# Optimization experiments

Hardware: AMD Instinct MI355X
Metric: run time of the kernel (lower is better)

## Reference

```python
import jax, jax.numpy as jnp
import numpy as np

MESH_SIZE = 0.01
TEMP = 0.001
T = 4096
HID = (16, 16, 16)


def _triangle_mesh():
    g = np.arange(-1.0, 1.0 + 1e-9, MESH_SIZE, dtype=np.float32)  # 201 pts
    A, B = np.meshgrid(g, g, indexing='ij')  # alpha rows, beta cols
    mask = A >= B                             # Preisach triangle alpha >= beta
    return A[mask].astype(np.float32), B[mask].astype(np.float32)  # [N], [N]


def _constrain(v, lo, hi):
    return lo + (hi - lo) * jax.nn.sigmoid(v)


def setup_inputs() -> dict:
    key = jax.random.key(0)
    ks = jax.random.split(key, 12)
    alpha_np, beta_np = _triangle_mesh()
    N = alpha_np.shape[0]  # 20301

    def xavier(k, fan_in, fan_out):
        b = np.sqrt(6.0 / (fan_in + fan_out)).astype(np.float32)
        return jax.random.uniform(k, (fan_in, fan_out), jnp.float32, -b, b)

    dims = (2,) + HID + (1,)
    params = {}
    for i in range(4):
        params[f'w{i+1}'] = xavier(ks[i], dims[i], dims[i + 1])
        params[f'b{i+1}'] = jnp.zeros((dims[i + 1],), jnp.float32)

    bound = np.sqrt(6.0 / (1 + N)).astype(np.float32)  # xavier_uniform on (1,N)
    init_state_raw = jax.random.uniform(ks[10], (N,), jnp.float32, -bound, bound)

    return dict(
        x=jax.random.normal(ks[11], (T,), jnp.float32),
        alpha_raw=jnp.asarray(alpha_np),
        beta_raw=jnp.asarray(beta_np),
        init_state_raw=init_state_raw,
        m_scale_raw=jnp.asarray(1.0, jnp.float32),
        m_offset_raw=jnp.asarray(1.0, jnp.float32),
        h_scale_raw=jnp.asarray(1.0, jnp.float32),
        **params,
    )


def _get_states(x, alpha, beta, s0, temp):
    # Soft Preisach relay: switch up where u>alpha, down where u<beta, else hold.
    def step(s, u):
        up = jax.nn.sigmoid((u - alpha) / temp)
        dn = jax.nn.sigmoid((beta - u) / temp)
        s_new = up - dn + (1.0 - up) * (1.0 - dn) * s
        return s_new, s_new
    _, states = jax.lax.scan(step, s0, x)
    return states  # [T, N]


def reference(x, alpha_raw, beta_raw, init_state_raw,
              w1, b1, w2, b2, w3, b3, w4, b4,
              m_scale_raw, m_offset_raw, h_scale_raw):
    alpha = alpha_raw  # ConstrainedParameter with no bounds -> identity
    beta = beta_raw
    s0 = jnp.tanh(init_state_raw)  # BinaryParameter (soft binary)

    states = _get_states(x, alpha, beta, s0, TEMP)  # [T, N]

    mesh = jnp.stack([alpha, beta], axis=1)  # [N, 2]
    h = jax.nn.relu(mesh @ w1 + b1)
    h = jax.nn.relu(h @ w2 + b2)
    h = jax.nn.relu(h @ w3 + b3)
    density = jax.nn.sigmoid(h @ w4 + b4)  # [N, 1]
    density = density.T  # [1, N]

    m = jnp.sum(density * states, axis=-1) / jnp.sum(density, axis=-1)  # [T]

    m_scale = _constrain(m_scale_raw, 0.0, 10.0)
    m_offset = _constrain(m_offset_raw, -10.0, 10.0)
    h_scale = _constrain(h_scale_raw, 0.0, 10.0)

    out = m_scale * m + m_offset + h_scale * x  # [T]
    return out, density, states
```

## Files before the change

kernel.cpp:

```cpp
#include <hip/hip_runtime.h>
#include <math.h>

#define NM 20301
#define TT 4096
#define NC 16
#define CH 256
#define NBLK 80
#define NWAVE 4
#define NPAR (NBLK*NWAVE)
#define TPH 16
#define NPH (CH / TPH)
#define LOG2E_K 1442.69504f
#define WNEAR 26.0f

__device__ __forceinline__ void relay_step(float ka, float kb, float ku,
                                           float& aa, float& bb) {
    float z1 = fminf(ka - ku, 63.f);
    float z2 = fminf(ku - kb, 63.f);
    float e1 = __builtin_amdgcn_exp2f(z1);
    float e2 = __builtin_amdgcn_exp2f(z2);
    float p1 = 1.f + e1, p2 = 1.f + e2;
    float r  = __builtin_amdgcn_rcpf(p1 * p2);
    aa = (e2 - e1) * r;
    bb = (e1 * e2) * r;
}

__device__ __forceinline__ float wave_reduce_sum(float w) {
    #pragma unroll
    for (int off = 32; off > 0; off >>= 1)
        w += __shfl_down(w, off, 64);
    return w;
}

__global__ __launch_bounds__(256) void density_kernel(
    const float* __restrict__ alpha, const float* __restrict__ beta,
    const float* __restrict__ w1, const float* __restrict__ b1,
    const float* __restrict__ w2, const float* __restrict__ b2,
    const float* __restrict__ w3, const float* __restrict__ b3,
    const float* __restrict__ w4, const float* __restrict__ b4,
    float* __restrict__ density_out, float* __restrict__ densum_parts)
{
    int n = blockIdx.x * 256 + threadIdx.x;
    bool valid = n < NM;
    int nn = valid ? n : NM - 1;
    float a = alpha[nn], b = beta[nn];

    float h1[16], h2[16], h3[16];
    #pragma unroll
    for (int j = 0; j < 16; j++) {
        float v = fmaf(a, w1[j], fmaf(b, w1[16 + j], b1[j]));
        h1[j] = fmaxf(v, 0.f);
    }
    #pragma unroll
    for (int j = 0; j < 16; j++) {
        float v = b2[j];
        #pragma unroll
        for (int k = 0; k < 16; k++) v = fmaf(h1[k], w2[k * 16 + j], v);
        h2[j] = fmaxf(v, 0.f);
    }
    #pragma unroll
    for (int j = 0; j < 16; j++) {
        float v = b3[j];
        #pragma unroll
        for (int k = 0; k < 16; k++) v = fmaf(h2[k], w3[k * 16 + j], v);
        h3[j] = fmaxf(v, 0.f);
    }
    float v = b4[0];
    #pragma unroll
    for (int k = 0; k < 16; k++) v = fmaf(h3[k], w4[k], v);
    float d = 1.f / (1.f + __expf(-v));

    if (valid) density_out[n] = d;
    float wsum = wave_reduce_sum(valid ? d : 0.f);
    __shared__ float ws_[NWAVE];
    if ((threadIdx.x & 63) == 0) ws_[threadIdx.x >> 6] = wsum;
    __syncthreads();
    if (threadIdx.x == 0)
        densum_parts[blockIdx.x] = ws_[0] + ws_[1] + ws_[2] + ws_[3];
}

__global__ __launch_bounds__(256) void chunk_compose_kernel(
    const float* __restrict__ x, const float* __restrict__ alpha,
    const float* __restrict__ beta,
    float* __restrict__ Abuf, float* __restrict__ Bbuf)
{
    __shared__ float xs[CH];
    int c = blockIdx.y;
    xs[threadIdx.x] = x[c * CH + threadIdx.x] * LOG2E_K;
    __syncthreads();

    int n = blockIdx.x * 256 + threadIdx.x;
    int nn = (n < NM) ? n : NM - 1;
    float ka = alpha[nn] * LOG2E_K;
    float kb = beta[nn] * LOG2E_K;

    float A = 0.f, B = 1.f;
    for (int p = 0; p < NPH; p++) {
        float xr[TPH];
        #pragma unroll
        for (int j = 0; j < TPH; j++) xr[j] = xs[p * TPH + j];
        #pragma unroll
        for (int j = 0; j < TPH; j++) {
            float ku = xr[j];
            float w1 = ka - ku, w2 = ku - kb;
            bool nearb = fminf(fabsf(w1), fabsf(w2)) < WNEAR;
            if (__any(nearb)) {
                float aa, bb;
                relay_step(ka, kb, ku, aa, bb);
                A = fmaf(bb, A, aa);
                B *= bb;
            } else {
                bool swu = w1 < 0.f, swd = w2 < 0.f;
                A = swu ? 1.f : (swd ? -1.f : A);
                B = (swu || swd) ? 0.f : B;
            }
        }
    }
    if (n < NM) { Abuf[c * NM + n] = A; Bbuf[c * NM + n] = B; }
}

__global__ __launch_bounds__(256) void chunk_scan_kernel(
    const float* __restrict__ init_raw,
    const float* __restrict__ Abuf, const float* __restrict__ Bbuf,
    float* __restrict__ sstart)
{
    int n = blockIdx.x * 256 + threadIdx.x;
    if (n >= NM) return;
    float s = tanhf(init_raw[n]);
    #pragma unroll
    for (int c = 0; c < NC; c++) {
        sstart[c * NM + n] = s;
        s = fmaf(Bbuf[c * NM + n], s, Abuf[c * NM + n]);
    }
}

__global__ __launch_bounds__(256) void states_kernel(
    const float* __restrict__ x, const float* __restrict__ alpha,
    const float* __restrict__ beta, const float* __restrict__ density,
    const float* __restrict__ sstart,
    float* __restrict__ states, float* __restrict__ partials)
{
    __shared__ float xs[CH];
    __shared__ float tile[NWAVE * 64 * (TPH + 1)];

    int tid = threadIdx.x;
    int c = blockIdx.y;
    xs[tid] = x[c * CH + tid] * LOG2E_K;

    int n = blockIdx.x * 256 + tid;
    bool valid = n < NM;
    int nn = valid ? n : NM - 1;
    float ka = alpha[nn] * LOG2E_K;
    float kb = beta[nn] * LOG2E_K;
    float d  = valid ? density[n] : 0.f;
    float s  = sstart[c * NM + nn];
    __syncthreads();

    int wv = tid >> 6, ln = tid & 63;
    int tl = ln & 15, h = ln >> 4;
    float* wtile = &tile[wv * 64 * (TPH + 1)];
    float* tslot = &wtile[ln * (TPH + 1)];
    float* rowp  = states + (size_t)c * CH * NM + n;
    size_t prow  = (size_t)(blockIdx.x * NWAVE + wv) * TT + c * CH;

    for (int p = 0; p < NPH; p++) {
        float xr[TPH];
        #pragma unroll
        for (int j = 0; j < TPH; j++) xr[j] = xs[p * TPH + j];
        #pragma unroll
        for (int j = 0; j < TPH; j++) {
            float ku = xr[j];
            float w1 = ka - ku, w2 = ku - kb;
            bool nearb = fminf(fabsf(w1), fabsf(w2)) < WNEAR;
            if (__any(nearb)) {
                float aa, bb;
                relay_step(ka, kb, ku, aa, bb);
                s = fmaf(bb, s, aa);
            } else {
                s = (w1 < 0.f) ? 1.f : ((w2 < 0.f) ? -1.f : s);
            }
            if (valid) rowp[(size_t)(p * TPH + j) * NM] = s;
            tslot[j] = d * s;
        }
        asm volatile("s_waitcnt lgkmcnt(0)" ::: "memory");
        float acc = 0.f;
        #pragma unroll
        for (int k = 0; k < TPH; k++)
            acc += wtile[(h * 16 + k) * (TPH + 1) + tl];
        acc += __shfl_xor(acc, 16, 64);
        acc += __shfl_xor(acc, 32, 64);
        if (ln < TPH) partials[prow + p * TPH + ln] = acc;
        asm volatile("s_waitcnt lgkmcnt(0)" ::: "memory");
    }
}

__global__ __launch_bounds__(256) void finalize_kernel(
    const float* __restrict__ x, const float* __restrict__ partials,
    const float* __restrict__ densum_parts,
    const float* __restrict__ msr, const float* __restrict__ mor,
    const float* __restrict__ hsr, float* __restrict__ out)
{
    int t = blockIdx.x * 256 + threadIdx.x;
    if (t >= TT) return;
    float acc = 0.f;
    for (int r = 0; r < NPAR; r++)
        acc += partials[(size_t)r * TT + t];
    float dsum = 0.f;
    for (int bx = 0; bx < NBLK; bx++)
        dsum += densum_parts[bx];
    float sig_ms = 1.f / (1.f + __expf(-msr[0]));
    float sig_mo = 1.f / (1.f + __expf(-mor[0]));
    float sig_hs = 1.f / (1.f + __expf(-hsr[0]));
    float m_scale  = 10.f * sig_ms;
    float m_offset = fmaf(20.f, sig_mo, -10.f);
    float h_scale  = 10.f * sig_hs;
    float m = acc / dsum;
    out[t] = fmaf(m_scale, m, m_offset) + h_scale * x[t];
}

extern "C" void kernel_launch(void* const* d_in, const int* in_sizes, int n_in,
                              void* d_out, int out_size, void* d_ws, size_t ws_size,
                              hipStream_t stream)
{
    const float* x    = (const float*)d_in[0];
    const float* alpha= (const float*)d_in[1];
    const float* beta = (const float*)d_in[2];
    const float* init = (const float*)d_in[3];
    const float* msr  = (const float*)d_in[4];
    const float* mor  = (const float*)d_in[5];
    const float* hsr  = (const float*)d_in[6];
    const float* w1   = (const float*)d_in[7];
    const float* b1   = (const float*)d_in[8];
    const float* w2   = (const float*)d_in[9];
    const float* b2   = (const float*)d_in[10];
    const float* w3   = (const float*)d_in[11];
    const float* b3   = (const float*)d_in[12];
    const float* w4   = (const float*)d_in[13];
    const float* b4   = (const float*)d_in[14];

    float* out     = (float*)d_out;
    float* density = out + TT;
    float* states  = density + NM;

    float* densum_parts = (float*)d_ws;
    float* sstart       = densum_parts + 128;
    float* partials     = sstart + NC * NM;

    float* Abuf = states;
    float* Bbuf = states + (size_t)NC * NM;

    density_kernel<<<dim3(NBLK), dim3(256), 0, stream>>>(
        alpha, beta, w1, b1, w2, b2, w3, b3, w4, b4, density, densum_parts);

    chunk_compose_kernel<<<dim3(NBLK, NC), dim3(256), 0, stream>>>(
        x, alpha, beta, Abuf, Bbuf);

    chunk_scan_kernel<<<dim3(NBLK), dim3(256), 0, stream>>>(
        init, Abuf, Bbuf, sstart);

    states_kernel<<<dim3(NBLK, NC), dim3(256), 0, stream>>>(
        x, alpha, beta, density, sstart, states, partials);

    finalize_kernel<<<dim3(TT / 256), dim3(256), 0, stream>>>(
        x, partials, densum_parts, msr, mor, hsr, out);
}
```

Baseline: 477.2 us.

## Re-split time into 256 short chunks with whole-mesh blocks for states pass

The time axis is split into 256 chunks of 16 steps instead of 16 chunks of 256. Each states block now covers one time chunk across the entire mesh, with 1024 threads holding 20 mesh points each. A row of states is written contiguously per step, and the density-weighted sum is reduced with wave shuffles instead of a shared-memory transpose. This aims to give a long-lived grid with coalesced full-row writes and fewer partials. In exchange, the chunk_scan pass becomes a 256-step sequential loop, the compose pass has many more small blocks, and the larger register arrays may lower occupancy.

```diff
diff --git a/kernel.cpp b/kernel.cpp
--- a/kernel.cpp
+++ b/kernel.cpp
@@ -3,13 +3,11 @@
 
 #define NM 20301
 #define TT 4096
-#define NC 16
-#define CH 256
+#define NCC 256
+#define CH2 16
 #define NBLK 80
-#define NWAVE 4
-#define NPAR (NBLK*NWAVE)
-#define TPH 16
-#define NPH (CH / TPH)
+#define NTH 1024
+#define KPT 20
 #define LOG2E_K 1442.69504f
 #define WNEAR 26.0f
 
@@ -72,7 +70,7 @@
 
     if (valid) density_out[n] = d;
     float wsum = wave_reduce_sum(valid ? d : 0.f);
-    __shared__ float ws_[NWAVE];
+    __shared__ float ws_[4];
     if ((threadIdx.x & 63) == 0) ws_[threadIdx.x >> 6] = wsum;
     __syncthreads();
     if (threadIdx.x == 0)
@@ -84,9 +82,9 @@
     const float* __restrict__ beta,
     float* __restrict__ Abuf, float* __restrict__ Bbuf)
 {
-    __shared__ float xs[CH];
+    __shared__ float xs[CH2];
     int c = blockIdx.y;
-    xs[threadIdx.x] = x[c * CH + threadIdx.x] * LOG2E_K;
+    if (threadIdx.x < CH2) xs[threadIdx.x] = x[c * CH2 + threadIdx.x] * LOG2E_K;
     __syncthreads();
 
     int n = blockIdx.x * 256 + threadIdx.x;
@@ -95,28 +93,23 @@
     float kb = beta[nn] * LOG2E_K;
 
     float A = 0.f, B = 1.f;
-    for (int p = 0; p < NPH; p++) {
-        float xr[TPH];
-        #pragma unroll
-        for (int j = 0; j < TPH; j++) xr[j] = xs[p * TPH + j];
-        #pragma unroll
-        for (int j = 0; j < TPH; j++) {
-            float ku = xr[j];
-            float w1 = ka - ku, w2 = ku - kb;
-            bool nearb = fminf(fabsf(w1), fabsf(w2)) < WNEAR;
-            if (__any(nearb)) {
-                float aa, bb;
-                relay_step(ka, kb, ku, aa, bb);
-                A = fmaf(bb, A, aa);
-                B *= bb;
-            } else {
-                bool swu = w1 < 0.f, swd = w2 < 0.f;
-                A = swu ? 1.f : (swd ? -1.f : A);
-                B = (swu || swd) ? 0.f : B;
-            }
+    #pragma unroll
+    for (int j = 0; j < CH2; j++) {
+        float ku = xs[j];
+        float w1 = ka - ku, w2 = ku - kb;
+        bool nearb = fminf(fabsf(w1), fabsf(w2)) < WNEAR;
+        if (__any(nearb)) {
+            float aa, bb;
+            relay_step(ka, kb, ku, aa, bb);
+            A = fmaf(bb, A, aa);
+            B *= bb;
+        } else {
+            bool swu = w1 < 0.f, swd = w2 < 0.f;
+            A = swu ? 1.f : (swd ? -1.f : A);
+            B = (swu || swd) ? 0.f : B;
         }
     }
-    if (n < NM) { Abuf[c * NM + n] = A; Bbuf[c * NM + n] = B; }
+    if (n < NM) { Abuf[(size_t)c * NM + n] = A; Bbuf[(size_t)c * NM + n] = B; }
 }
 
 __global__ __launch_bounds__(256) void chunk_scan_kernel(
@@ -127,84 +120,78 @@
     int n = blockIdx.x * 256 + threadIdx.x;
     if (n >= NM) return;
     float s = tanhf(init_raw[n]);
-    #pragma unroll
-    for (int c = 0; c < NC; c++) {
-        sstart[c * NM + n] = s;
-        s = fmaf(Bbuf[c * NM + n], s, Abuf[c * NM + n]);
-    }
-}
-
-__global__ __launch_bounds__(256) void states_kernel(
+    #pragma unroll 4
+    for (int c = 0; c < NCC; c++) {
+        sstart[(size_t)c * NM + n] = s;
+        s = fmaf(Bbuf[(size_t)c * NM + n], s, Abuf[(size_t)c * NM + n]);
+    }
+}
+
+__global__ __launch_bounds__(NTH) void states_kernel(
     const float* __restrict__ x, const float* __restrict__ alpha,
     const float* __restrict__ beta, const float* __restrict__ density,
     const float* __restrict__ sstart,
-    float* __restrict__ states, float* __restrict__ partials)
-{
-    __shared__ float xs[CH];
-    __shared__ float tile[NWAVE * 64 * (TPH + 1)];
-
+    float* __restrict__ states, float* __restrict__ wpart)
+{
+    __shared__ float xsh[CH2];
+    int b = blockIdx.x;
     int tid = threadIdx.x;
-    int c = blockIdx.y;
-    xs[tid] = x[c * CH + tid] * LOG2E_K;
-
-    int n = blockIdx.x * 256 + tid;
-    bool valid = n < NM;
-    int nn = valid ? n : NM - 1;
-    float ka = alpha[nn] * LOG2E_K;
-    float kb = beta[nn] * LOG2E_K;
-    float d  = valid ? density[n] : 0.f;
-    float s  = sstart[c * NM + nn];
+    if (tid < CH2) xsh[tid] = x[b * CH2 + tid] * LOG2E_K;
+
+    float s_reg[KPT], d_reg[KPT], ka[KPT], kb[KPT];
+    #pragma unroll
+    for (int k = 0; k < KPT; k++) {
+        int n = tid + NTH * k;
+        bool v = n < NM;
+        int nn = v ? n : NM - 1;
+        ka[k] = alpha[nn] * LOG2E_K;
+        kb[k] = beta[nn] * LOG2E_K;
+        d_reg[k] = v ? density[n] : 0.f;
+        s_reg[k] = sstart[(size_t)b * NM + nn];
+    }
     __syncthreads();
 
-    int wv = tid >> 6, ln = tid & 63;
-    int tl = ln & 15, h = ln >> 4;
-    float* wtile = &tile[wv * 64 * (TPH + 1)];
-    float* tslot = &wtile[ln * (TPH + 1)];
-    float* rowp  = states + (size_t)c * CH * NM + n;
-    size_t prow  = (size_t)(blockIdx.x * NWAVE + wv) * TT + c * CH;
-
-    for (int p = 0; p < NPH; p++) {
-        float xr[TPH];
+    int wv = tid >> 6;
+    for (int t = 0; t < CH2; t++) {
+        float u = xsh[t];
+        float* __restrict__ row = states + (size_t)(b * CH2 + t) * NM;
+        float acc = 0.f;
         #pragma unroll
-        for (int j = 0; j < TPH; j++) xr[j] = xs[p * TPH + j];
-        #pragma unroll
-        for (int j = 0; j < TPH; j++) {
-            float ku = xr[j];
-            float w1 = ka - ku, w2 = ku - kb;
+        for (int k = 0; k < KPT; k++) {
+            int n = tid + NTH * k;
+            float w1 = ka[k] - u, w2 = u - kb[k];
+            float s = s_reg[k];
             bool nearb = fminf(fabsf(w1), fabsf(w2)) < WNEAR;
             if (__any(nearb)) {
                 float aa, bb;
-                relay_step(ka, kb, ku, aa, bb);
+                relay_step(ka[k], kb[k], u, aa, bb);
                 s = fmaf(bb, s, aa);
             } else {
                 s = (w1 < 0.f) ? 1.f : ((w2 < 0.f) ? -1.f : s);
             }
-            if (valid) rowp[(size_t)(p * TPH + j) * NM] = s;
-            tslot[j] = d * s;
+            s_reg[k] = s;
+            if (n < NM) row[n] = s;
+            acc = fmaf(d_reg[k], s, acc);
         }
-        asm volatile("s_waitcnt lgkmcnt(0)" ::: "memory");
-        float acc = 0.f;
-        #pragma unroll
-        for (int k = 0; k < TPH; k++)
-            acc += wtile[(h * 16 + k) * (TPH + 1) + tl];
-        acc += __shfl_xor(acc, 16, 64);
-        acc += __shfl_xor(acc, 32, 64);
-        if (ln < TPH) partials[prow + p * TPH + ln] = acc;
-        asm volatile("s_waitcnt lgkmcnt(0)" ::: "memory");
+        acc = wave_reduce_sum(acc);
+        if ((tid & 63) == 0)
+            wpart[(size_t)(b * 16 + wv) * CH2 + t] = acc;
     }
 }
 
 __global__ __launch_bounds__(256) void finalize_kernel(
-    const float* __restrict__ x, const float* __restrict__ partials,
+    const float* __restrict__ x, const float* __restrict__ wpart,
     const float* __restrict__ densum_parts,
     const float* __restrict__ msr, const float* __restrict__ mor,
     const float* __restrict__ hsr, float* __restrict__ out)
 {
     int t = blockIdx.x * 256 + threadIdx.x;
     if (t >= TT) return;
+    int b = t >> 4, tl = t & 15;
     float acc = 0.f;
-    for (int r = 0; r < NPAR; r++)
-        acc += partials[(size_t)r * TT + t];
+    #pragma unroll
+    for (int w = 0; w < 16; w++)
+        acc += wpart[(size_t)(b * 16 + w) * CH2 + tl];
     float dsum = 0.f;
     for (int bx = 0; bx < NBLK; bx++)
         dsum += densum_parts[bx];
@@ -244,23 +231,23 @@
 
     float* densum_parts = (float*)d_ws;
     float* sstart       = densum_parts + 128;
-    float* partials     = sstart + NC * NM;
+    float* wpart        = sstart + (size_t)NCC * NM;
 
     float* Abuf = states;
-    float* Bbuf = states + (size_t)NC * NM;
+    float* Bbuf = states + (size_t)NCC * NM;
 
     density_kernel<<<dim3(NBLK), dim3(256), 0, stream>>>(
         alpha, beta, w1, b1, w2, b2, w3, b3, w4, b4, density, densum_parts);
 
-    chunk_compose_kernel<<<dim3(NBLK, NC), dim3(256), 0, stream>>>(
+    chunk_compose_kernel<<<dim3(NBLK, NCC), dim3(256), 0, stream>>>(
         x, alpha, beta, Abuf, Bbuf);
 
     chunk_scan_kernel<<<dim3(NBLK), dim3(256), 0, stream>>>(
         init, Abuf, Bbuf, sstart);
 
-    states_kernel<<<dim3(NBLK, NC), dim3(256), 0, stream>>>(
-        x, alpha, beta, density, sstart, states, partials);
+    states_kernel<<<dim3(NCC), dim3(NTH), 0, stream>>>(
+        x, alpha, beta, density, sstart, states, wpart);
 
     finalize_kernel<<<dim3(TT / 256), dim3(256), 0, stream>>>(
-        x, partials, densum_parts, msr, mor, hsr, out);
-}
+        x, wpart, densum_parts, msr, mor, hsr, out);
+}
```

Measured after the change: 482.4 us. Within noise of the previous version (+1.1%).

## Halve time chunk length and process two relay columns per thread in states kernel

Applied to the files above, without the earlier changes.

Time is now split into 32 chunks of 128 steps instead of 16 of 256, so each chunk-compose and states thread runs a shorter serial chain over more blocks. The states kernel gives each thread two mesh columns, so the x-loads and the wave-level near-threshold branch test are shared across twice the work and each block writes half as many density-weighted partials. In exchange the chunk-scan pass is twice as long, there is more register pressure, and a wave now takes the expensive sigmoid path whenever either of its two columns is near a threshold.

```diff
diff --git a/kernel.cpp b/kernel.cpp
--- a/kernel.cpp
+++ b/kernel.cpp
@@ -3,11 +3,11 @@
 
 #define NM 20301
 #define TT 4096
-#define NC 16
-#define CH 256
+#define NC 32
+#define CH 128
 #define NBLK 80
-#define NWAVE 4
-#define NPAR (NBLK*NWAVE)
+#define SBLK 40
+#define NPROW (SBLK * 4)
 #define TPH 16
 #define NPH (CH / TPH)
 #define LOG2E_K 1442.69504f
@@ -72,7 +72,7 @@
 
     if (valid) density_out[n] = d;
     float wsum = wave_reduce_sum(valid ? d : 0.f);
-    __shared__ float ws_[NWAVE];
+    __shared__ float ws_[4];
     if ((threadIdx.x & 63) == 0) ws_[threadIdx.x >> 6] = wsum;
     __syncthreads();
     if (threadIdx.x == 0)
@@ -86,7 +86,7 @@
 {
     __shared__ float xs[CH];
     int c = blockIdx.y;
-    xs[threadIdx.x] = x[c * CH + threadIdx.x] * LOG2E_K;
+    if (threadIdx.x < CH) xs[threadIdx.x] = x[c * CH + threadIdx.x] * LOG2E_K;
     __syncthreads();
 
     int n = blockIdx.x * 256 + threadIdx.x;
@@ -102,21 +102,21 @@
         #pragma unroll
         for (int j = 0; j < TPH; j++) {
             float ku = xr[j];
-            float w1 = ka - ku, w2 = ku - kb;
-            bool nearb = fminf(fabsf(w1), fabsf(w2)) < WNEAR;
+            float d1 = ka - ku, d2 = ku - kb;
+            bool nearb = fminf(fabsf(d1), fabsf(d2)) < WNEAR;
             if (__any(nearb)) {
                 float aa, bb;
                 relay_step(ka, kb, ku, aa, bb);
                 A = fmaf(bb, A, aa);
                 B *= bb;
             } else {
-                bool swu = w1 < 0.f, swd = w2 < 0.f;
-                A = swu ? 1.f : (swd ? -1.f : A);
-                B = (swu || swd) ? 0.f : B;
+                bool su = d1 < 0.f, sd = d2 < 0.f;
+                A = su ? 1.f : (sd ? -1.f : A);
+                B = (su || sd) ? 0.f : B;
             }
         }
     }
-    if (n < NM) { Abuf[c * NM + n] = A; Bbuf[c * NM + n] = B; }
+    if (n < NM) { Abuf[(size_t)c * NM + n] = A; Bbuf[(size_t)c * NM + n] = B; }
 }
 
 __global__ __launch_bounds__(256) void chunk_scan_kernel(
@@ -127,10 +127,10 @@
     int n = blockIdx.x * 256 + threadIdx.x;
     if (n >= NM) return;
     float s = tanhf(init_raw[n]);
-    #pragma unroll
+    #pragma unroll 4
     for (int c = 0; c < NC; c++) {
-        sstart[c * NM + n] = s;
-        s = fmaf(Bbuf[c * NM + n], s, Abuf[c * NM + n]);
+        sstart[(size_t)c * NM + n] = s;
+        s = fmaf(Bbuf[(size_t)c * NM + n], s, Abuf[(size_t)c * NM + n]);
     }
 }
 
@@ -141,27 +141,30 @@
     float* __restrict__ states, float* __restrict__ partials)
 {
     __shared__ float xs[CH];
-    __shared__ float tile[NWAVE * 64 * (TPH + 1)];
+    __shared__ float tile[4 * 64 * (TPH + 1)];
 
     int tid = threadIdx.x;
     int c = blockIdx.y;
-    xs[tid] = x[c * CH + tid] * LOG2E_K;
-
-    int n = blockIdx.x * 256 + tid;
-    bool valid = n < NM;
-    int nn = valid ? n : NM - 1;
-    float ka = alpha[nn] * LOG2E_K;
-    float kb = beta[nn] * LOG2E_K;
-    float d  = valid ? density[n] : 0.f;
-    float s  = sstart[c * NM + nn];
+    if (tid < CH) xs[tid] = x[c * CH + tid] * LOG2E_K;
+
+    int n0 = blockIdx.x * 512 + tid;
+    int n1 = n0 + 256;
+    bool v0 = n0 < NM, v1 = n1 < NM;
+    int nn0 = v0 ? n0 : NM - 1, nn1 = v1 ? n1 : NM - 1;
+    float ka0 = alpha[nn0] * LOG2E_K, kb0 = beta[nn0] * LOG2E_K;
+    float ka1 = alpha[nn1] * LOG2E_K, kb1 = beta[nn1] * LOG2E_K;
+    float d0 = v0 ? density[n0] : 0.f, d1 = v1 ? density[n1] : 0.f;
+    float s0 = sstart[(size_t)c * NM + nn0];
+    float s1 = sstart[(size_t)c * NM + nn1];
     __syncthreads();
 
     int wv = tid >> 6, ln = tid & 63;
     int tl = ln & 15, h = ln >> 4;
     float* wtile = &tile[wv * 64 * (TPH + 1)];
     float* tslot = &wtile[ln * (TPH + 1)];
-    float* rowp  = states + (size_t)c * CH * NM + n;
-    size_t prow  = (size_t)(blockIdx.x * NWAVE + wv) * TT + c * CH;
+    float* rowp0 = states + (size_t)c * CH * NM + n0;
+    float* rowp1 = states + (size_t)c * CH * NM + n1;
+    size_t prow  = (size_t)(blockIdx.x * 4 + wv) * TT + c * CH;
 
     for (int p = 0; p < NPH; p++) {
         float xr[TPH];
@@ -169,18 +172,25 @@
         for (int j = 0; j < TPH; j++) xr[j] = xs[p * TPH + j];
         #pragma unroll
         for (int j = 0; j < TPH; j++) {
-            float ku = xr[j];
-            float w1 = ka - ku, w2 = ku - kb;
-            bool nearb = fminf(fabsf(w1), fabsf(w2)) < WNEAR;
-            if (__any(nearb)) {
+            float u = xr[j];
+            float w10 = ka0 - u, w20 = u - kb0;
+            float w11 = ka1 - u, w21 = u - kb1;
+            float near0 = fminf(fabsf(w10), fabsf(w20));
+            float near1 = fminf(fabsf(w11), fabsf(w21));
+            if (__any(fminf(near0, near1) < WNEAR)) {
                 float aa, bb;
-                relay_step(ka, kb, ku, aa, bb);
-                s = fmaf(bb, s, aa);
+                relay_step(ka0, kb0, u, aa, bb);
+                s0 = fmaf(bb, s0, aa);
+                relay_step(ka1, kb1, u, aa, bb);
+                s1 = fmaf(bb, s1, aa);
             } else {
-                s = (w1 < 0.f) ? 1.f : ((w2 < 0.f) ? -1.f : s);
+                s0 = (w10 < 0.f) ? 1.f : ((w20 < 0.f) ? -1.f : s0);
+                s1 = (w11 < 0.f) ? 1.f : ((w21 < 0.f) ? -1.f : s1);
             }
-            if (valid) rowp[(size_t)(p * TPH + j) * NM] = s;
-            tslot[j] = d * s;
+            size_t roff = (size_t)(p * TPH + j) * NM;
+            if (v0) rowp0[roff] = s0;
+            if (v1) rowp1[roff] = s1;
+            tslot[j] = fmaf(d0, s0, d1 * s1);
         }
         asm volatile("s_waitcnt lgkmcnt(0)" ::: "memory");
         float acc = 0.f;
@@ -203,7 +213,7 @@
     int t = blockIdx.x * 256 + threadIdx.x;
     if (t >= TT) return;
     float acc = 0.f;
-    for (int r = 0; r < NPAR; r++)
+    for (int r = 0; r < NPROW; r++)
         acc += partials[(size_t)r * TT + t];
     float dsum = 0.f;
     for (int bx = 0; bx < NBLK; bx++)
@@ -244,7 +254,7 @@
 
     float* densum_parts = (float*)d_ws;
     float* sstart       = densum_parts + 128;
-    float* partials     = sstart + NC * NM;
+    float* partials     = sstart + (size_t)NC * NM;
 
     float* Abuf = states;
     float* Bbuf = states + (size_t)NC * NM;
@@ -258,7 +268,7 @@
     chunk_scan_kernel<<<dim3(NBLK), dim3(256), 0, stream>>>(
         init, Abuf, Bbuf, sstart);
 
-    states_kernel<<<dim3(NBLK, NC), dim3(256), 0, stream>>>(
+    states_kernel<<<dim3(SBLK, NC), dim3(256), 0, stream>>>(
         x, alpha, beta, density, sstart, states, partials);
 
     finalize_kernel<<<dim3(TT / 256), dim3(256), 0, stream>>>(
```

Result: faster. 455.2 us (-4.6%).
